# Performance work log

Measured on AMD Instinct MI355X. Metric: run time of the kernel, lower is better.

## Reference

```python
import jax, jax.numpy as jnp
import numpy as np

B, H, F, Z = 256, 2048, 1024, 512
T, PREV, TS = 16, 16, 32  # predicted_visit, previous_visit, time_step


def _relu_dense(x, W, b):
    return jax.nn.relu(x @ W + b)


def setup_inputs() -> dict:
    key = jax.random.key(0)
    ks = jax.random.split(key, 40)
    def rn(i, shape, scale=0.02):
        return jax.random.normal(ks[i], shape, jnp.float32) * scale
    D = H + F + Z  # LSTM input dim: concat(z_j, h_i, y_j_)
    inp = {
        'h_i': jax.random.normal(ks[0], (B, H), jnp.float32),
        # increasing visit times so Hawkes exp(past - current) stays bounded
        'input_t': jnp.cumsum(jax.random.uniform(ks[1], (B, TS), jnp.float32), axis=1) * 0.1,
        'Wk': rn(2, (D, 4 * H)),
        'Wr': rn(3, (H, 4 * H)),
        'b_lstm': jnp.zeros((4 * H,), jnp.float32),
    }
    dense_dims = [(H, F), (F, F), (F, F), (2 * H + 2 * F, Z), (Z, Z), (Z, Z), (2 * H + F, Z), (Z, Z), (Z, Z)]
    for n, (di, do) in enumerate(dense_dims, start=1):
        inp['W%d' % n] = rn(3 + n, (di, do))
        inp['b%d' % n] = jnp.zeros((do,), jnp.float32)
    for n, name in enumerate(['alpha', 'beta', 'base', 'tw']):
        inp[name] = jax.random.uniform(ks[20 + n], (1, 1), jnp.float32) * 0.05
    inp['noise_inf'] = jax.random.normal(ks[30], (T, B, Z), jnp.float32)
    inp['noise_prior'] = jax.random.normal(ks[31], (T, B, Z), jnp.float32)
    return inp


def reference(h_i, input_t, Wk, Wr, b_lstm, W1, b1, W2, b2, W3, b3, W4, b4, W5, b5, W6, b6, W7, b7, W8, b8, W9, b9, alpha, beta, base, tw, noise_inf, noise_prior):
    # ---- Hawkes intensity for every decode step (vectorized over steps) ----
    idxs = PREV + jnp.arange(T)                        # current_time_index per step j
    cur_t = input_t[:, idxs]                           # [B, T]
    diff = input_t[:, None, :] - cur_t[:, :, None]     # [B, T, TS] = past - current
    mask = jnp.arange(TS)[None, None, :] < idxs[None, :, None]
    trig = jnp.sum(jnp.where(mask, jnp.exp(diff), 0.0), axis=-1)   # [B, T]
    lam = base[0, 0] + alpha[0, 0] * beta[0, 0] * trig             # conditional intensity [B, T]
    # original: softplus(matmul(tile(lam,[1,H]), tile(tw,[H,1]))) == softplus(lam * H * tw)
    delta_t = jnp.log1p(jnp.exp(lam * (H * tw[0, 0])))             # [B, T]
    time_est = cur_t + delta_t                                     # [B, T]

    def step(carry, xs):
        h, c, y_prev, z_prev = carry
        lam_j, n_inf, n_pri = xs
        x = jnp.concatenate([z_prev, h_i, y_prev], axis=1)         # [B, Z+H+F]
        gates = x @ Wk + h @ Wr + b_lstm                           # [B, 4H]
        i_g, f_g, g_g, o_g = jnp.split(gates, 4, axis=1)           # keras gate order i,f,c,o
        c_new = jax.nn.sigmoid(f_g) * c + jax.nn.sigmoid(i_g) * jnp.tanh(g_g)
        h_new = jax.nn.sigmoid(o_g) * jnp.tanh(c_new)
        # Original code indexes keras state as c=state[0](=h_new), h_=state[1](=c_new):
        # s_j fed to the VAE nets is the CELL state, and the intensity scales the cell
        # that is carried to the next step, while h carried is the unscaled h_new.
        s_j = c_new
        c_next = lam_j[:, None] * c_new
        y = _relu_dense(_relu_dense(_relu_dense(h_new, W1, b1), W2, b2), W3, b3)
        hz = _relu_dense(jnp.concatenate([h_i, s_j, y, y_prev], axis=1), W4, b4)
        mean = _relu_dense(hz, W5, b5)
        logv = _relu_dense(hz, W6, b6)
        z = mean + n_inf * jnp.sqrt(jnp.exp(logv))
        hz_p = _relu_dense(jnp.concatenate([h_i, s_j, y_prev], axis=1), W7, b7)
        mean_p = _relu_dense(hz_p, W8, b8)
        logv_p = _relu_dense(hz_p, W9, b9)
        z_p = mean_p + n_pri * jnp.sqrt(jnp.exp(logv_p))
        return (h_new, c_next, y, z), (y, mean, logv, z, z_p)

    carry0 = (jnp.zeros((B, H), h_i.dtype), jnp.zeros((B, H), h_i.dtype),
              jnp.zeros((B, F), h_i.dtype), jnp.zeros((B, Z), h_i.dtype))
    xs = (lam.T, noise_inf, noise_prior)  # leading axis = decode step
    _, (ys, means, logvs, zs, zps) = jax.lax.scan(step, carry0, xs)
    tb = lambda a: jnp.transpose(a, (1, 0, 2))    # [T,B,*] -> [B,T,*]
    input_t_all = cur_t.T.reshape(-1, 1)          # matches per-step concat of [B,1]
    time_estimates = time_est.T.reshape(-1, 1)
    return (tb(ys), tb(means), tb(logvs), tb(zs), tb(zps), input_t_all, time_estimates)
```

## Files before the change

### kernel.cpp

```cpp
#include <hip/hip_runtime.h>
#include <stdint.h>

typedef unsigned short u16;
typedef __bf16 bf16x8 __attribute__((ext_vector_type(8)));
typedef float f32x4 __attribute__((ext_vector_type(4)));

static constexpr int NB  = 256;
static constexpr int NH  = 2048;
static constexpr int NF  = 1024;
static constexpr int NZ  = 512;
static constexpr int NT  = 16;
static constexpr int NTS = 32;
static constexpr int NG4 = 8192;
static constexpr int NBLK = 256;

__device__ __forceinline__ u16 f2bf(float f) {
  union { float f; uint32_t u; } x; x.f = f;
  uint32_t r = x.u + 0x7fffu + ((x.u >> 16) & 1u);
  return (u16)(r >> 16);
}
__device__ __forceinline__ float sigm(float x) { return 1.f / (1.f + expf(-x)); }

__device__ __forceinline__ void gload16(const void* g, void* l) {
  __builtin_amdgcn_global_load_lds(
      (__attribute__((address_space(1))) void*)const_cast<void*>(g),
      (__attribute__((address_space(3))) void*)l, 16, 0, 0);
}

__device__ __forceinline__ unsigned aload(const unsigned* p) {
  return __hip_atomic_load(p, __ATOMIC_RELAXED, __HIP_MEMORY_SCOPE_AGENT);
}
__device__ __forceinline__ void astore(unsigned* p, unsigned v) {
  __hip_atomic_store(p, v, __ATOMIC_RELAXED, __HIP_MEMORY_SCOPE_AGENT);
}
__device__ __forceinline__ void t_st(float* p, float v) {
  __hip_atomic_store(p, v, __ATOMIC_RELAXED, __HIP_MEMORY_SCOPE_AGENT);
}
__device__ __forceinline__ void t_st32(uint32_t* p, uint32_t v) {
  __hip_atomic_store(p, v, __ATOMIC_RELAXED, __HIP_MEMORY_SCOPE_AGENT);
}
__device__ __forceinline__ void t_stu16(u16* p, u16 v) {
  __hip_atomic_store(p, v, __ATOMIC_RELAXED, __HIP_MEMORY_SCOPE_AGENT);
}

__device__ __forceinline__ void tl4(const float* p, f32x4& v) {
  asm volatile("global_load_dwordx4 %0, %1, off sc0 sc1" : "=&v"(v) : "v"(p));
}
__device__ __forceinline__ void ts2(void* p, uint32_t lo, uint32_t hi) {
  uint2 d; d.x = lo; d.y = hi;
  asm volatile("global_store_dwordx2 %0, %1, off sc0 sc1" :: "v"(p), "v"(d) : "memory");
}
__device__ __forceinline__ void t_wait() {
  asm volatile("s_waitcnt vmcnt(0)" ::: "memory");
  __builtin_amdgcn_sched_barrier(0);
}

__device__ __forceinline__ void gsync(unsigned* flags, unsigned* rel, unsigned& epoch) {
  ++epoch;
  asm volatile("s_waitcnt vmcnt(0)" ::: "memory");
  __syncthreads();
  if (blockIdx.x == 0) {
    if (threadIdx.x > 0)
      while (aload(&flags[threadIdx.x]) < epoch) __builtin_amdgcn_s_sleep(1);
    __syncthreads();
    if (threadIdx.x == 0) astore(rel, epoch);
  } else if (threadIdx.x == 0) {
    astore(&flags[blockIdx.x], epoch);
    while (aload(rel) < epoch) __builtin_amdgcn_s_sleep(1);
  }
  __syncthreads();
}

template<int F>
__device__ __forceinline__ void gemm_core(const u16* __restrict__ A, const u16* __restrict__ W,
                                          int lda, int ldw, int niter, int wg,
                                          char* lds, f32x4 (&acc)[F][4]) {
  constexpr int BUF = F * 4096 + 4096;
  const int tid = threadIdx.x, lane = tid & 63, wave = tid >> 6;
  const int srow = lane >> 2;
  const int schunk = (((lane & 3) ^ ((lane >> 3) & 3)) << 3);
  const u16* ga = A + (size_t)(wave * (F * 16) + srow) * lda + schunk;
  const u16* gw = W + (size_t)(wave * wg + srow) * ldw + schunk;
  const size_t astep = (size_t)16 * lda;
  auto STAGE = [&](int idx) {
    const int koff = idx << 5;
    char* base = lds + (idx % 3) * BUF;
    char* ad = base + wave * (F * 1024);
#pragma unroll
    for (int k = 0; k < F; ++k) gload16(ga + koff + k * astep, ad + k * 1024);
    gload16(gw + koff, base + F * 4096 + wave * 1024);
  };
  int rA[F], rW[4];
  const int b15 = lane & 15, h4 = lane >> 4, rx = (b15 >> 1) & 3;
#pragma unroll
  for (int f = 0; f < F; ++f) rA[f] = (wave * (F * 16) + f * 16 + b15) * 64 + ((h4 ^ rx) << 4);
#pragma unroll
  for (int q = 0; q < 4; ++q) rW[q] = F * 4096 + (q * 16 + b15) * 64 + ((h4 ^ rx) << 4);

  const int npro = niter < 3 ? niter : 3;
  for (int j = 0; j < npro; ++j) STAGE(j);
  for (int i = 0; i < niter; ++i) {
    const int ahead = niter - 1 - i;
    if constexpr (F == 4) {
      if (ahead >= 2)      asm volatile("s_waitcnt vmcnt(10)" ::: "memory");
      else if (ahead == 1) asm volatile("s_waitcnt vmcnt(5)" ::: "memory");
      else                 asm volatile("s_waitcnt vmcnt(0)" ::: "memory");
    } else if constexpr (F == 2) {
      if (ahead >= 2)      asm volatile("s_waitcnt vmcnt(6)" ::: "memory");
      else if (ahead == 1) asm volatile("s_waitcnt vmcnt(3)" ::: "memory");
      else                 asm volatile("s_waitcnt vmcnt(0)" ::: "memory");
    } else {
      if (ahead >= 2)      asm volatile("s_waitcnt vmcnt(4)" ::: "memory");
      else if (ahead == 1) asm volatile("s_waitcnt vmcnt(2)" ::: "memory");
      else                 asm volatile("s_waitcnt vmcnt(0)" ::: "memory");
    }
    __builtin_amdgcn_sched_barrier(0);
    asm volatile("s_barrier" ::: "memory");
    __builtin_amdgcn_sched_barrier(0);
    const char* base = lds + (i % 3) * BUF;
    bf16x8 av[F], bv[4];
#pragma unroll
    for (int f = 0; f < F; ++f) av[f] = *(const bf16x8*)(base + rA[f]);
#pragma unroll
    for (int q = 0; q < 4; ++q) bv[q] = *(const bf16x8*)(base + rW[q]);
    asm volatile("s_waitcnt lgkmcnt(0)" ::: "memory");
    __builtin_amdgcn_sched_barrier(0);
    asm volatile("s_barrier" ::: "memory");
    __builtin_amdgcn_sched_barrier(0);
    if (i + 3 < niter) STAGE(i + 3);
#pragma unroll
    for (int f = 0; f < F; ++f)
#pragma unroll
      for (int q = 0; q < 4; ++q)
        acc[f][q] = __builtin_amdgcn_mfma_f32_16x16x32_bf16(av[f], bv[q], acc[f][q], 0, 0, 0);
  }
}

__device__ __forceinline__ void wpart1(float* P, int m0, int n0, const f32x4 (&acc)[1][4]) {
  const int tid = threadIdx.x, lane = tid & 63, wave = tid >> 6;
  const int b15 = lane & 15, h4 = lane >> 4;
#pragma unroll
  for (int q = 0; q < 4; ++q) {
    const int n = n0 + q * 16 + b15;
#pragma unroll
    for (int r = 0; r < 4; ++r) {
      const int ml = wave * 16 + h4 * 4 + r;
      t_st(&P[(size_t)(m0 + ml) * 512 + n], acc[0][q][r]);
    }
  }
}

__device__ __forceinline__ void wbias(float* of, const float* bias, int Nn, int n0,
                                      const f32x4 (&acc)[4][4]) {
  const int tid = threadIdx.x, lane = tid & 63, wave = tid >> 6;
  const int b15 = lane & 15, h4 = lane >> 4;
#pragma unroll
  for (int q = 0; q < 4; ++q) {
    const int n = n0 + q * 16 + b15;
    const float bb = bias[n];
#pragma unroll
    for (int f = 0; f < 4; ++f) {
      const int m = wave * 64 + f * 16 + h4 * 4;
#pragma unroll
      for (int r = 0; r < 4; ++r) t_st(&of[(size_t)(m + r) * Nn + n], acc[f][q][r] + bb);
    }
  }
}

struct TJobs {
  const float* W[13]; u16* D[13];
  int N[13], klo[13], ntx[13], base[14];
  const float* h_i; u16* hi_bf; int hi_base;
};
__global__ __launch_bounds__(256) void setup_tr(TJobs j) {
  const int bid = blockIdx.x, t = threadIdx.x;
  if (bid >= j.hi_base) {
    int i = ((bid - j.hi_base) * 256 + t) * 4;
    float4 v = *(const float4*)(j.h_i + i);
    ushort4 o; o.x = f2bf(v.x); o.y = f2bf(v.y); o.z = f2bf(v.z); o.w = f2bf(v.w);
    *(ushort4*)(j.hi_bf + i) = o;
    return;
  }
  int k = 0;
  while (bid >= j.base[k + 1]) ++k;
  const int tix = bid - j.base[k];
  const int ntx = j.ntx[k];
  const int kk0 = (tix % ntx) * 32, n0 = (tix / ntx) * 32;
  const int N = j.N[k], k_lo = j.klo[k], k_len = ntx * 32;
  const float* W = j.W[k];
  u16* WT = j.D[k];
  __shared__ float tile[32][33];
  const int r = t >> 3, cg = t & 7;
  const float4 v = *(const float4*)(W + (size_t)(k_lo + kk0 + r) * N + n0 + cg * 4);
  tile[r][cg * 4 + 0] = v.x; tile[r][cg * 4 + 1] = v.y;
  tile[r][cg * 4 + 2] = v.z; tile[r][cg * 4 + 3] = v.w;
  __syncthreads();
  ushort4 o;
  o.x = f2bf(tile[cg * 4 + 0][r]);
  o.y = f2bf(tile[cg * 4 + 1][r]);
  o.z = f2bf(tile[cg * 4 + 2][r]);
  o.w = f2bf(tile[cg * 4 + 3][r]);
  *(ushort4*)(WT + (size_t)(n0 + r) * k_len + kk0 + cg * 4) = o;
}

__global__ __launch_bounds__(256) void misc_k(const float* __restrict__ input_t,
                                              const float* alpha, const float* beta,
                                              const float* base_, const float* tw,
                                              const float* b5, const float* b6,
                                              const float* b8, const float* b9,
                                              float* __restrict__ lam_buf,
                                              float* __restrict__ out_it,
                                              float* __restrict__ out_te,
                                              float* __restrict__ bq) {
  const int bid = blockIdx.x, tid = threadIdx.x;
  if (bid < 16) {
    int i = bid * 256 + tid;
    int b = i >> 4, jj = i & 15;
    const float* row = input_t + b * NTS;
    float cur = row[16 + jj];
    float trig = 0.f;
    int lim = 16 + jj;
    for (int s = 0; s < lim; ++s) trig += expf(row[s] - cur);
    float lam = base_[0] + alpha[0] * beta[0] * trig;
    float x = lam * (2048.f * tw[0]);
    float dt = (x > 15.f) ? x : log1pf(expf(x));
    lam_buf[b * NT + jj] = lam;
    out_it[jj * NB + b] = cur;
    out_te[jj * NB + b] = cur + dt;
  } else {
    int i = (bid - 16) * 256 + tid;
    bq[i] = (i < 512) ? b5[i] : (i < 1024) ? b6[i - 512]
          : (i < 1536) ? b8[i - 1024] : b9[i - 1536];
  }
}

struct PArgs {
  const u16 *WkzT, *WkyT, *WkmT, *WrT, *W1T, *W2T, *W3T, *W4T, *W56T, *W7T, *W89T, *hi_bf;
  const float *bl, *b1, *b2, *b3, *b4, *b7, *bq, *ninf, *npri, *lam;
  float *Gc, *H4c, *H7c, *R;
  u16 *hbfV, *zV, *yV, *sbfV, *y1V, *y2V, *hzV, *hzpV;
  float *o_ys, *o_mean, *o_logv, *o_zs, *o_zps;
  unsigned *flags, *rel;
};

__global__ __launch_bounds__(256) void persist(PArgs a) {
  __shared__ __attribute__((aligned(16))) char lds[3 * 20480];
  const int bid = blockIdx.x, tid = threadIdx.x;
  const int lane = tid & 63, wave = tid >> 6, b15 = lane & 15, h4 = lane >> 4;
  unsigned epoch = 0;
  float* Q    = a.R;
  float* Phz  = a.R + (size_t)4 * NB * 512;
  float* Phzp = a.R + (size_t)8 * NB * 512;

  const int g_mh = bid >> 7;
  const int g_c0 = (bid & 127) * 16;
  float cR[2][4];
#pragma unroll
  for (int f = 0; f < 2; ++f)
#pragma unroll
    for (int r = 0; r < 4; ++r) cR[f][r] = 0.f;

  {
    if (bid < 144) {
      f32x4 acc[4][4] = {};
      if (bid < 128) {
        const int n0 = bid * 64;
        gemm_core<4>(a.hi_bf, a.WkmT + (size_t)n0 * 2048, 2048, 2048, 64, 16, lds, acc);
        wbias(a.Gc, a.bl, NG4, n0, acc);
      } else if (bid < 136) {
        const int n0 = (bid - 128) * 64;
        gemm_core<4>(a.hi_bf, a.W4T + (size_t)n0 * 6144, 2048, 6144, 64, 16, lds, acc);
        wbias(a.H4c, a.b4, NZ, n0, acc);
      } else {
        const int n0 = (bid - 136) * 64;
        gemm_core<4>(a.hi_bf, a.W7T + (size_t)n0 * 5120, 2048, 5120, 64, 16, lds, acc);
        wbias(a.H7c, a.b7, NZ, n0, acc);
      }
    } else {
      const int zt = (bid - 144) * 256 + tid, nthr = 112 * 256;
      for (int w = zt; w < NB * NH / 2; w += nthr) t_st32((uint32_t*)a.hbfV + w, 0u);
      for (int w = zt; w < NB * NZ / 2; w += nthr) t_st32((uint32_t*)a.zV + w, 0u);
      for (int w = zt; w < NB * NF / 2; w += nthr) t_st32((uint32_t*)a.yV + w, 0u);
    }
    gsync(a.flags, a.rel, epoch);
  }

  float GcR[2][4][4];
#pragma unroll
  for (int f = 0; f < 2; ++f)
#pragma unroll
    for (int q = 0; q < 4; ++q)
#pragma unroll
      for (int r = 0; r < 4; ++r) {
        const int m = g_mh * 128 + wave * 32 + f * 16 + h4 * 4 + r;
        GcR[f][q][r] = a.Gc[(size_t)m * NG4 + q * 2048 + g_c0 + b15];
      }

  for (int t = 0; t < NT; ++t) {
    const u16* hbf_t = a.hbfV + (size_t)t * NB * NH;
    u16* hbf_n = a.hbfV + (size_t)(t + 1) * NB * NH;
    const u16* z_t = a.zV + (size_t)t * NB * NZ;
    u16* z_n = a.zV + (size_t)(t + 1) * NB * NZ;
    const u16* yp = a.yV + (size_t)t * NB * NF;
    u16* yc = a.yV + (size_t)(t + 1) * NB * NF;
    u16* sbf = a.sbfV + (size_t)t * NB * NH;
    u16* y1bf = a.y1V + (size_t)t * NB * NF;
    u16* y2bf = a.y2V + (size_t)t * NB * NF;
    u16* hzbf = a.hzV + (size_t)t * NB * NZ;
    u16* hzpbf = a.hzpV + (size_t)t * NB * NZ;

    {
      f32x4 acc[2][4] = {};
      gemm_core<2>(z_t + (size_t)g_mh * 128 * 512, a.WkzT + (size_t)g_c0 * 512,
                   512, 512, 16, 2048, lds, acc);
      gemm_core<2>(yp + (size_t)g_mh * 128 * 1024, a.WkyT + (size_t)g_c0 * 1024,
                   1024, 1024, 32, 2048, lds, acc);
      gemm_core<2>(hbf_t + (size_t)g_mh * 128 * 2048, a.WrT + (size_t)g_c0 * 2048,
                   2048, 2048, 64, 2048, lds, acc);
      __syncthreads();
      u16* tlh = (u16*)lds;
      u16* tls = (u16*)(lds + 4096);
#pragma unroll
      for (int f = 0; f < 2; ++f)
#pragma unroll
        for (int r = 0; r < 4; ++r) {
          const int ml = wave * 32 + f * 16 + h4 * 4 + r;
          const int m = g_mh * 128 + ml;
          const float ig = acc[f][0][r] + GcR[f][0][r];
          const float fg = acc[f][1][r] + GcR[f][1][r];
          const float gg = acc[f][2][r] + GcR[f][2][r];
          const float og = acc[f][3][r] + GcR[f][3][r];
          const float cn = sigm(fg) * cR[f][r] + sigm(ig) * tanhf(gg);
          const float hn = sigm(og) * tanhf(cn);
          cR[f][r] = a.lam[m * NT + t] * cn;
          tlh[ml * 16 + b15] = f2bf(hn);
          tls[ml * 16 + b15] = f2bf(cn);
        }
      __syncthreads();
      {
        const int row = tid >> 1, half = tid & 1;
        const char* srch = lds + row * 32 + half * 16;
        uint2 u0 = *(const uint2*)srch;
        uint2 u1 = *(const uint2*)(srch + 8);
        u16* dh = hbf_n + (size_t)(g_mh * 128 + row) * NH + g_c0 + half * 8;
        ts2(dh, u0.x, u0.y);
        ts2(dh + 4, u1.x, u1.y);
        const char* srcs = lds + 4096 + row * 32 + half * 16;
        uint2 s0 = *(const uint2*)srcs;
        uint2 s1 = *(const uint2*)(srcs + 8);
        u16* dsp = sbf + (size_t)(g_mh * 128 + row) * NH + g_c0 + half * 8;
        ts2(dsp, s0.x, s0.y);
        ts2(dsp + 4, s1.x, s1.y);
      }
      gsync(a.flags, a.rel, epoch);
    }

    {
      if (bid < 64) {
        const int mt = bid >> 4, nt = bid & 15, m0 = mt * 64, n0 = nt * 64;
        f32x4 acc[1][4] = {};
        gemm_core<1>(hbf_n + (size_t)m0 * 2048, a.W1T + (size_t)n0 * 2048,
                     2048, 2048, 64, 16, lds, acc);
#pragma unroll
        for (int q = 0; q < 4; ++q) {
          const int n = n0 + q * 16 + b15;
          const float bb = a.b1[n];
#pragma unroll
          for (int r = 0; r < 4; ++r) {
            const int ml = wave * 16 + h4 * 4 + r;
            t_stu16(&y1bf[(size_t)(m0 + ml) * NF + n], f2bf(fmaxf(acc[0][q][r] + bb, 0.f)));
          }
        }
      } else if (bid < 128) {
        const int s = bid - 64, mt = s >> 4, rest = s & 15, nt = rest & 7, k = rest >> 3;
        const int m0 = mt * 64, n0 = nt * 64;
        f32x4 acc[1][4] = {};
        gemm_core<1>(sbf + (size_t)m0 * 2048 + k * 1024,
                     a.W4T + 2048 + (size_t)n0 * 6144 + k * 1024,
                     2048, 6144, 32, 16, lds, acc);
        wpart1(Phz + (size_t)k * NB * 512, m0, n0, acc);
      } else if (bid < 160) {
        const int s = bid - 128, mt = s >> 3, nt = s & 7, m0 = mt * 64, n0 = nt * 64;
        f32x4 acc[1][4] = {};
        gemm_core<1>(yp + (size_t)m0 * 1024, a.W4T + 5120 + (size_t)n0 * 6144,
                     1024, 6144, 32, 16, lds, acc);
        wpart1(Phz + (size_t)2 * NB * 512, m0, n0, acc);
      } else if (bid < 224) {
        const int s = bid - 160, mt = s >> 4, rest = s & 15, nt = rest & 7, k = rest >> 3;
        const int m0 = mt * 64, n0 = nt * 64;
        f32x4 acc[1][4] = {};
        gemm_core<1>(sbf + (size_t)m0 * 2048 + k * 1024,
                     a.W7T + 2048 + (size_t)n0 * 5120 + k * 1024,
                     2048, 5120, 32, 16, lds, acc);
        wpart1(Phzp + (size_t)k * NB * 512, m0, n0, acc);
      } else {
        const int s = bid - 224, mt = s >> 3, nt = s & 7, m0 = mt * 64, n0 = nt * 64;
        f32x4 acc[1][4] = {};
        gemm_core<1>(yp + (size_t)m0 * 1024, a.W7T + 4096 + (size_t)n0 * 5120,
                     1024, 5120, 32, 16, lds, acc);
        wpart1(Phzp + (size_t)2 * NB * 512, m0, n0, acc);
      }
      gsync(a.flags, a.rel, epoch);
    }

    {
      if (bid < 64) {
        const int mt = bid >> 4, nt = bid & 15, m0 = mt * 64, n0 = nt * 64;
        f32x4 acc[1][4] = {};
        gemm_core<1>(y1bf + (size_t)m0 * 1024, a.W2T + (size_t)n0 * 1024,
                     1024, 1024, 32, 16, lds, acc);
#pragma unroll
        for (int q = 0; q < 4; ++q) {
          const int n = n0 + q * 16 + b15;
          const float bb = a.b2[n];
#pragma unroll
          for (int r = 0; r < 4; ++r) {
            const int ml = wave * 16 + h4 * 4 + r;
            t_stu16(&y2bf[(size_t)(m0 + ml) * NF + n], f2bf(fmaxf(acc[0][q][r] + bb, 0.f)));
          }
        }
      } else if (bid < 96) {
        const int cb = bid - 64;
        for (int p = 0; p < 4; ++p) {
          const int idx = ((p * 32 + cb) * 256 + tid) * 4;
          f32x4 v0, v1, v2;
          tl4(Phzp + idx, v0);
          tl4(Phzp + (size_t)NB * 512 + idx, v1);
          tl4(Phzp + (size_t)2 * NB * 512 + idx, v2);
          f32x4 c0 = *(const f32x4*)(a.H7c + idx);
          t_wait();
          f32x4 v = v0 + v1 + v2 + c0;
          u16 o[4];
#pragma unroll
          for (int r = 0; r < 4; ++r) o[r] = f2bf(fmaxf(v[r], 0.f));
          ts2(hzpbf + idx, (uint32_t)o[0] | ((uint32_t)o[1] << 16),
                           (uint32_t)o[2] | ((uint32_t)o[3] << 16));
        }
      }
      gsync(a.flags, a.rel, epoch);
    }

    {
      if (bid < 64) {
        const int mt = bid >> 4, nt = bid & 15, m0 = mt * 64, n0 = nt * 64;
        f32x4 acc[1][4] = {};
        gemm_core<1>(y2bf + (size_t)m0 * 1024, a.W3T + (size_t)n0 * 1024,
                     1024, 1024, 32, 16, lds, acc);
#pragma unroll
        for (int q = 0; q < 4; ++q) {
          const int n = n0 + q * 16 + b15;
          const float bb = a.b3[n];
#pragma unroll
          for (int r = 0; r < 4; ++r) {
            const int ml = wave * 16 + h4 * 4 + r;
            const float v = fmaxf(acc[0][q][r] + bb, 0.f);
            t_stu16(&yc[(size_t)(m0 + ml) * NF + n], f2bf(v));
            a.o_ys[((size_t)(m0 + ml) * NT + t) * NF + n] = v;
          }
        }
      } else if (bid < 128) {
        const int s = bid - 64, mt = s >> 4, nt = s & 15, m0 = mt * 64, n0 = nt * 64;
        f32x4 acc[1][4] = {};
        gemm_core<1>(hzpbf + (size_t)m0 * 512, a.W89T + (size_t)n0 * 512,
                     512, 512, 16, 16, lds, acc);
#pragma unroll
        for (int q = 0; q < 4; ++q) {
          const int n = n0 + q * 16 + b15;
          const int plane = 2 + (n >> 9), col = n & 511;
          const float bb = a.bq[1024 + n];
#pragma unroll
          for (int r = 0; r < 4; ++r) {
            const int ml = wave * 16 + h4 * 4 + r;
            t_st(&Q[(size_t)plane * NB * 512 + (size_t)(m0 + ml) * 512 + col],
                 fmaxf(acc[0][q][r] + bb, 0.f));
          }
        }
      }
      gsync(a.flags, a.rel, epoch);
    }

    {
      if (bid < 32) {
        const int mt = bid >> 3, nt = bid & 7, m0 = mt * 64, n0 = nt * 64;
        f32x4 acc[1][4] = {};
        gemm_core<1>(yc + (size_t)m0 * 1024, a.W4T + 4096 + (size_t)n0 * 6144,
                     1024, 6144, 32, 16, lds, acc);
        wpart1(Phz + (size_t)3 * NB * 512, m0, n0, acc);
      }
      gsync(a.flags, a.rel, epoch);
    }

    {
      if (bid < 32) {
        for (int p = 0; p < 4; ++p) {
          const int idx = ((p * 32 + bid) * 256 + tid) * 4;
          f32x4 v0, v1, v2, v3;
          tl4(Phz + idx, v0);
          tl4(Phz + (size_t)NB * 512 + idx, v1);
          tl4(Phz + (size_t)2 * NB * 512 + idx, v2);
          tl4(Phz + (size_t)3 * NB * 512 + idx, v3);
          f32x4 c0 = *(const f32x4*)(a.H4c + idx);
          t_wait();
          f32x4 v = v0 + v1 + v2 + v3 + c0;
          u16 o[4];
#pragma unroll
          for (int r = 0; r < 4; ++r) o[r] = f2bf(fmaxf(v[r], 0.f));
          ts2(hzbf + idx, (uint32_t)o[0] | ((uint32_t)o[1] << 16),
                          (uint32_t)o[2] | ((uint32_t)o[3] << 16));
        }
      }
      gsync(a.flags, a.rel, epoch);
    }

    {
      if (bid < 64) {
        const int mt = bid >> 4, nt = bid & 15, m0 = mt * 64, n0 = nt * 64;
        f32x4 acc[1][4] = {};
        gemm_core<1>(hzbf + (size_t)m0 * 512, a.W56T + (size_t)n0 * 512,
                     512, 512, 16, 16, lds, acc);
#pragma unroll
        for (int q = 0; q < 4; ++q) {
          const int n = n0 + q * 16 + b15;
          const int plane = n >> 9, col = n & 511;
          const float bb = a.bq[n];
#pragma unroll
          for (int r = 0; r < 4; ++r) {
            const int ml = wave * 16 + h4 * 4 + r;
            t_st(&Q[(size_t)plane * NB * 512 + (size_t)(m0 + ml) * 512 + col],
                 fmaxf(acc[0][q][r] + bb, 0.f));
          }
        }
      }
      gsync(a.flags, a.rel, epoch);
    }

    {
      if (bid < 128) {
        const int g2 = bid * 256 + tid;
        const int i = g2 * 4, m = i >> 9, jj = i & 511;
        const float* qb = Q + (size_t)m * 512 + jj;
        f32x4 mean, logv, mpv, lpv;
        tl4(qb, mean);
        tl4(qb + (size_t)NB * 512, logv);
        tl4(qb + (size_t)2 * NB * 512, mpv);
        tl4(qb + (size_t)3 * NB * 512, lpv);
        f32x4 nI = *(const f32x4*)(a.ninf + (size_t)t * NB * NZ + i);
        f32x4 nP = *(const f32x4*)(a.npri + (size_t)t * NB * NZ + i);
        t_wait();
        f32x4 z, zp;
        u16 zq[4];
#pragma unroll
        for (int r = 0; r < 4; ++r) {
          z[r] = fmaf(nI[r], sqrtf(expf(logv[r])), mean[r]);
          zp[r] = fmaf(nP[r], sqrtf(expf(lpv[r])), mpv[r]);
          zq[r] = f2bf(z[r]);
        }
        const size_t oo = ((size_t)m * NT + t) * NZ + jj;
        *(f32x4*)(a.o_mean + oo) = mean;
        *(f32x4*)(a.o_logv + oo) = logv;
        *(f32x4*)(a.o_zs + oo) = z;
        *(f32x4*)(a.o_zps + oo) = zp;
        ts2(z_n + i, (uint32_t)zq[0] | ((uint32_t)zq[1] << 16),
                     (uint32_t)zq[2] | ((uint32_t)zq[3] << 16));
      }
      gsync(a.flags, a.rel, epoch);
    }
  }
}

extern "C" void kernel_launch(void* const* d_in, const int* in_sizes, int n_in,
                              void* d_out, int out_size, void* d_ws, size_t ws_size,
                              hipStream_t stream) {
  const float* h_i  = (const float*)d_in[0];
  const float* in_t = (const float*)d_in[1];
  const float* Wk   = (const float*)d_in[2];
  const float* Wr   = (const float*)d_in[3];
  const float* bl   = (const float*)d_in[4];
  const float* W1 = (const float*)d_in[5];  const float* b1 = (const float*)d_in[6];
  const float* W2 = (const float*)d_in[7];  const float* b2 = (const float*)d_in[8];
  const float* W3 = (const float*)d_in[9];  const float* b3 = (const float*)d_in[10];
  const float* W4 = (const float*)d_in[11]; const float* b4 = (const float*)d_in[12];
  const float* W5 = (const float*)d_in[13]; const float* b5 = (const float*)d_in[14];
  const float* W6 = (const float*)d_in[15]; const float* b6 = (const float*)d_in[16];
  const float* W7 = (const float*)d_in[17]; const float* b7 = (const float*)d_in[18];
  const float* W8 = (const float*)d_in[19]; const float* b8 = (const float*)d_in[20];
  const float* W9 = (const float*)d_in[21]; const float* b9 = (const float*)d_in[22];
  const float* alpha = (const float*)d_in[23];
  const float* beta  = (const float*)d_in[24];
  const float* base_ = (const float*)d_in[25];
  const float* tw    = (const float*)d_in[26];
  const float* ninf  = (const float*)d_in[27];
  const float* npri  = (const float*)d_in[28];
  float* out = (float*)d_out;
  (void)in_sizes; (void)n_in; (void)out_size; (void)ws_size;

  char* wsb = (char*)d_ws;
  size_t off = 0;
  auto alloc = [&](size_t bytes) -> void* {
    void* p = wsb + off;
    off += (bytes + 255) & ~(size_t)255;
    return p;
  };
  u16* WkzT = (u16*)alloc((size_t)NG4 * 512 * 2);
  u16* WkmT = (u16*)alloc((size_t)NG4 * 2048 * 2);
  u16* WkyT = (u16*)alloc((size_t)NG4 * 1024 * 2);
  u16* WrT  = (u16*)alloc((size_t)NG4 * NH * 2);
  u16* W1T  = (u16*)alloc((size_t)NF * NH * 2);
  u16* W2T  = (u16*)alloc((size_t)NF * NF * 2);
  u16* W3T  = (u16*)alloc((size_t)NF * NF * 2);
  u16* W4T  = (u16*)alloc((size_t)NZ * 6144 * 2);
  u16* W56T = (u16*)alloc((size_t)1024 * NZ * 2);
  u16* W7T  = (u16*)alloc((size_t)NZ * 5120 * 2);
  u16* W89T = (u16*)alloc((size_t)1024 * NZ * 2);
  u16* hi_bf = (u16*)alloc((size_t)NB * NH * 2);
  float* bq  = (float*)alloc(2048 * 4);
  float* Gc  = (float*)alloc((size_t)NB * NG4 * 4);
  float* H4c = (float*)alloc((size_t)NB * NZ * 4);
  float* H7c = (float*)alloc((size_t)NB * NZ * 4);
  float* lam = (float*)alloc((size_t)NB * NT * 4);
  u16* hbfV = (u16*)alloc((size_t)(NT + 1) * NB * NH * 2);
  u16* zV   = (u16*)alloc((size_t)(NT + 1) * NB * NZ * 2);
  u16* yV   = (u16*)alloc((size_t)(NT + 1) * NB * NF * 2);
  u16* sbfV = (u16*)alloc((size_t)NT * NB * NH * 2);
  u16* y1V  = (u16*)alloc((size_t)NT * NB * NF * 2);
  u16* y2V  = (u16*)alloc((size_t)NT * NB * NF * 2);
  u16* hzV  = (u16*)alloc((size_t)NT * NB * NZ * 2);
  u16* hzpV = (u16*)alloc((size_t)NT * NB * NZ * 2);
  char* zero_start = wsb + off;
  unsigned* bar = (unsigned*)alloc(2048);
  size_t zero_bytes = (size_t)((wsb + off) - zero_start);

  float* out_ys   = out;
  float* out_mean = out_ys + (size_t)NB * NT * NF;
  float* out_logv = out_mean + (size_t)NB * NT * NZ;
  float* out_zs   = out_logv + (size_t)NB * NT * NZ;
  float* out_zps  = out_zs + (size_t)NB * NT * NZ;
  float* out_it   = out_zps + (size_t)NB * NT * NZ;
  float* out_te   = out_it + (size_t)NB * NT;

  hipMemsetAsync(zero_start, 0, zero_bytes, stream);

  TJobs tj{};
  const float* srcs[13] = {Wk, Wk, Wk, Wr, W1, W2, W3, W4, W5, W6, W7, W8, W9};
  u16* dsts[13] = {WkzT, WkmT, WkyT, WrT, W1T, W2T, W3T, W4T,
                   W56T, W56T + (size_t)NZ * NZ, W7T, W89T, W89T + (size_t)NZ * NZ};
  int Ns[13]   = {8192, 8192, 8192, 8192, 1024, 1024, 1024, 512, 512, 512, 512, 512, 512};
  int klos[13] = {0, 512, 2560, 0, 0, 0, 0, 0, 0, 0, 0, 0, 0};
  int klens[13]= {512, 2048, 1024, 2048, 2048, 1024, 1024, 6144, 512, 512, 5120, 512, 512};
  int cum = 0;
  for (int k = 0; k < 13; ++k) {
    tj.W[k] = srcs[k]; tj.D[k] = dsts[k]; tj.N[k] = Ns[k]; tj.klo[k] = klos[k];
    tj.ntx[k] = klens[k] / 32;
    tj.base[k] = cum;
    cum += (klens[k] / 32) * (Ns[k] / 32);
  }
  tj.base[13] = cum;
  tj.h_i = h_i; tj.hi_bf = hi_bf; tj.hi_base = cum;
  const int total_blocks = cum + (NB * NH / 4) / 256;
  setup_tr<<<dim3(total_blocks), dim3(256), 0, stream>>>(tj);

  misc_k<<<dim3(24), dim3(256), 0, stream>>>(in_t, alpha, beta, base_, tw,
                                             b5, b6, b8, b9, lam, out_it, out_te, bq);

  PArgs pa{};
  pa.WkzT = WkzT; pa.WkyT = WkyT; pa.WkmT = WkmT; pa.WrT = WrT;
  pa.W1T = W1T; pa.W2T = W2T; pa.W3T = W3T; pa.W4T = W4T;
  pa.W56T = W56T; pa.W7T = W7T; pa.W89T = W89T; pa.hi_bf = hi_bf;
  pa.bl = bl; pa.b1 = b1; pa.b2 = b2; pa.b3 = b3; pa.b4 = b4; pa.b7 = b7;
  pa.bq = bq; pa.ninf = ninf; pa.npri = npri; pa.lam = lam;
  pa.Gc = Gc; pa.H4c = H4c; pa.H7c = H7c; pa.R = (float*)WkmT;
  pa.hbfV = hbfV; pa.zV = zV; pa.yV = yV; pa.sbfV = sbfV;
  pa.y1V = y1V; pa.y2V = y2V; pa.hzV = hzV; pa.hzpV = hzpV;
  pa.o_ys = out_ys; pa.o_mean = out_mean; pa.o_logv = out_logv;
  pa.o_zs = out_zs; pa.o_zps = out_zps;
  pa.flags = bar; pa.rel = bar + 384;
  persist<<<dim3(NBLK), dim3(256), 0, stream>>>(pa);
}
```

Baseline: 1.726 ms.

## Fuse reduction and reparameterization epilogues into GEMM phases, removing two grid syncs

The W8/W9 prior GEMM now has each block compute both the mean and logvar tiles for the same columns and write z_p directly. The W4 partial-sum reduction plus ReLU is moved into the last hz GEMM's epilogue. The W5/W6 GEMM emits mean, logv, z and the bf16 z feedback in place. This drops the Q staging buffer and two grid-wide barriers per decode step. In exchange fewer blocks are active in those phases (32 instead of 64/128), and outputs are written with scalar rather than vectorized stores.

```diff
diff --git a/kernel.cpp b/kernel.cpp
--- a/kernel.cpp
+++ b/kernel.cpp
@@ -32,6 +32,9 @@
 }
 __device__ __forceinline__ void astore(unsigned* p, unsigned v) {
   __hip_atomic_store(p, v, __ATOMIC_RELAXED, __HIP_MEMORY_SCOPE_AGENT);
+}
+__device__ __forceinline__ float t_ld(const float* p) {
+  return __hip_atomic_load(p, __ATOMIC_RELAXED, __HIP_MEMORY_SCOPE_AGENT);
 }
 __device__ __forceinline__ void t_st(float* p, float v) {
   __hip_atomic_store(p, v, __ATOMIC_RELAXED, __HIP_MEMORY_SCOPE_AGENT);
@@ -248,7 +251,6 @@
   const int bid = blockIdx.x, tid = threadIdx.x;
   const int lane = tid & 63, wave = tid >> 6, b15 = lane & 15, h4 = lane >> 4;
   unsigned epoch = 0;
-  float* Q    = a.R;
   float* Phz  = a.R + (size_t)4 * NB * 512;
   float* Phzp = a.R + (size_t)8 * NB * 512;
 
@@ -458,21 +460,24 @@
             a.o_ys[((size_t)(m0 + ml) * NT + t) * NF + n] = v;
           }
         }
-      } else if (bid < 128) {
-        const int s = bid - 64, mt = s >> 4, nt = s & 15, m0 = mt * 64, n0 = nt * 64;
-        f32x4 acc[1][4] = {};
-        gemm_core<1>(hzpbf + (size_t)m0 * 512, a.W89T + (size_t)n0 * 512,
-                     512, 512, 16, 16, lds, acc);
+      } else if (bid < 96) {
+        const int s = bid - 64, mt = s >> 3, nt = s & 7, m0 = mt * 64, jj0 = nt * 64;
+        f32x4 accM[1][4] = {}, accL[1][4] = {};
+        gemm_core<1>(hzpbf + (size_t)m0 * 512, a.W89T + (size_t)jj0 * 512,
+                     512, 512, 16, 16, lds, accM);
+        gemm_core<1>(hzpbf + (size_t)m0 * 512, a.W89T + (size_t)(512 + jj0) * 512,
+                     512, 512, 16, 16, lds, accL);
 #pragma unroll
         for (int q = 0; q < 4; ++q) {
-          const int n = n0 + q * 16 + b15;
-          const int plane = 2 + (n >> 9), col = n & 511;
-          const float bb = a.bq[1024 + n];
+          const int jj = jj0 + q * 16 + b15;
+          const float bm = a.bq[1024 + jj], bv = a.bq[1536 + jj];
 #pragma unroll
           for (int r = 0; r < 4; ++r) {
-            const int ml = wave * 16 + h4 * 4 + r;
-            t_st(&Q[(size_t)plane * NB * 512 + (size_t)(m0 + ml) * 512 + col],
-                 fmaxf(acc[0][q][r] + bb, 0.f));
+            const int row = m0 + wave * 16 + h4 * 4 + r;
+            const float mp = fmaxf(accM[0][q][r] + bm, 0.f);
+            const float lp = fmaxf(accL[0][q][r] + bv, 0.f);
+            const float nP = a.npri[(size_t)t * NB * NZ + (size_t)row * NZ + jj];
+            a.o_zps[((size_t)row * NT + t) * NZ + jj] = fmaf(nP, sqrtf(expf(lp)), mp);
           }
         }
       }
@@ -485,83 +490,50 @@
         f32x4 acc[1][4] = {};
         gemm_core<1>(yc + (size_t)m0 * 1024, a.W4T + 4096 + (size_t)n0 * 6144,
                      1024, 6144, 32, 16, lds, acc);
-        wpart1(Phz + (size_t)3 * NB * 512, m0, n0, acc);
+#pragma unroll
+        for (int q = 0; q < 4; ++q) {
+          const int n = n0 + q * 16 + b15;
+#pragma unroll
+          for (int r = 0; r < 4; ++r) {
+            const int row = m0 + wave * 16 + h4 * 4 + r;
+            const size_t idx = (size_t)row * 512 + n;
+            float v = acc[0][q][r] + t_ld(Phz + idx)
+                    + t_ld(Phz + (size_t)NB * 512 + idx)
+                    + t_ld(Phz + (size_t)2 * NB * 512 + idx)
+                    + a.H4c[idx];
+            t_stu16(&hzbf[idx], f2bf(fmaxf(v, 0.f)));
+          }
+        }
       }
       gsync(a.flags, a.rel, epoch);
     }
 
     {
       if (bid < 32) {
-        for (int p = 0; p < 4; ++p) {
-          const int idx = ((p * 32 + bid) * 256 + tid) * 4;
-          f32x4 v0, v1, v2, v3;
-          tl4(Phz + idx, v0);
-          tl4(Phz + (size_t)NB * 512 + idx, v1);
-          tl4(Phz + (size_t)2 * NB * 512 + idx, v2);
-          tl4(Phz + (size_t)3 * NB * 512 + idx, v3);
-          f32x4 c0 = *(const f32x4*)(a.H4c + idx);
-          t_wait();
-          f32x4 v = v0 + v1 + v2 + v3 + c0;
-          u16 o[4];
-#pragma unroll
-          for (int r = 0; r < 4; ++r) o[r] = f2bf(fmaxf(v[r], 0.f));
-          ts2(hzbf + idx, (uint32_t)o[0] | ((uint32_t)o[1] << 16),
-                          (uint32_t)o[2] | ((uint32_t)o[3] << 16));
-        }
-      }
-      gsync(a.flags, a.rel, epoch);
-    }
-
-    {
-      if (bid < 64) {
-        const int mt = bid >> 4, nt = bid & 15, m0 = mt * 64, n0 = nt * 64;
-        f32x4 acc[1][4] = {};
-        gemm_core<1>(hzbf + (size_t)m0 * 512, a.W56T + (size_t)n0 * 512,
-                     512, 512, 16, 16, lds, acc);
+        const int mt = bid >> 3, nt = bid & 7, m0 = mt * 64, jj0 = nt * 64;
+        f32x4 accM[1][4] = {}, accL[1][4] = {};
+        gemm_core<1>(hzbf + (size_t)m0 * 512, a.W56T + (size_t)jj0 * 512,
+                     512, 512, 16, 16, lds, accM);
+        gemm_core<1>(hzbf + (size_t)m0 * 512, a.W56T + (size_t)(512 + jj0) * 512,
+                     512, 512, 16, 16, lds, accL);
 #pragma unroll
         for (int q = 0; q < 4; ++q) {
-          const int n = n0 + q * 16 + b15;
-          const int plane = n >> 9, col = n & 511;
-          const float bb = a.bq[n];
+          const int jj = jj0 + q * 16 + b15;
+          const float bm = a.bq[jj], bv = a.bq[512 + jj];
 #pragma unroll
           for (int r = 0; r < 4; ++r) {
-            const int ml = wave * 16 + h4 * 4 + r;
-            t_st(&Q[(size_t)plane * NB * 512 + (size_t)(m0 + ml) * 512 + col],
-                 fmaxf(acc[0][q][r] + bb, 0.f));
+            const int row = m0 + wave * 16 + h4 * 4 + r;
+            const float mean = fmaxf(accM[0][q][r] + bm, 0.f);
+            const float logv = fmaxf(accL[0][q][r] + bv, 0.f);
+            const float nI = a.ninf[(size_t)t * NB * NZ + (size_t)row * NZ + jj];
+            const float z = fmaf(nI, sqrtf(expf(logv)), mean);
+            const size_t oo = ((size_t)row * NT + t) * NZ + jj;
+            a.o_mean[oo] = mean;
+            a.o_logv[oo] = logv;
+            a.o_zs[oo] = z;
+            t_stu16(&z_n[(size_t)row * NZ + jj], f2bf(z));
           }
         }
-      }
-      gsync(a.flags, a.rel, epoch);
-    }
-
-    {
-      if (bid < 128) {
-        const int g2 = bid * 256 + tid;
-        const int i = g2 * 4, m = i >> 9, jj = i & 511;
-        const float* qb = Q + (size_t)m * 512 + jj;
-        f32x4 mean, logv, mpv, lpv;
-        tl4(qb, mean);
-        tl4(qb + (size_t)NB * 512, logv);
-        tl4(qb + (size_t)2 * NB * 512, mpv);
-        tl4(qb + (size_t)3 * NB * 512, lpv);
-        f32x4 nI = *(const f32x4*)(a.ninf + (size_t)t * NB * NZ + i);
-        f32x4 nP = *(const f32x4*)(a.npri + (size_t)t * NB * NZ + i);
-        t_wait();
-        f32x4 z, zp;
-        u16 zq[4];
-#pragma unroll
-        for (int r = 0; r < 4; ++r) {
-          z[r] = fmaf(nI[r], sqrtf(expf(logv[r])), mean[r]);
-          zp[r] = fmaf(nP[r], sqrtf(expf(lpv[r])), mpv[r]);
-          zq[r] = f2bf(z[r]);
-        }
-        const size_t oo = ((size_t)m * NT + t) * NZ + jj;
-        *(f32x4*)(a.o_mean + oo) = mean;
-        *(f32x4*)(a.o_logv + oo) = logv;
-        *(f32x4*)(a.o_zs + oo) = z;
-        *(f32x4*)(a.o_zps + oo) = zp;
-        ts2(z_n + i, (uint32_t)zq[0] | ((uint32_t)zq[1] << 16),
-                     (uint32_t)zq[2] | ((uint32_t)zq[3] << 16));
       }
       gsync(a.flags, a.rel, epoch);
     }
```

Measured after the change: 2.231 ms. +29.2%, slower.
